# Performance work log

Measured on AMD Instinct MI355X. Metric: run time of the kernel, lower is better.

The kernel has to match this reference:

```python
import jax, jax.numpy as jnp
import numpy as np

N_NODES = 100000
N_EDGES = 1200000
D = 64
EPS = 1e-7
BETA = 1.0


def setup_inputs() -> dict:
    key = jax.random.key(0)
    k1, k2, k3, k4, k5 = jax.random.split(key, 5)
    node_feats = jax.random.normal(k1, (N_NODES, D), dtype=jnp.float32)
    edge_feats = jax.random.normal(k2, (N_EDGES, D), dtype=jnp.float32)
    W = jax.random.normal(k3, (D, D), dtype=jnp.float32) * (1.0 / np.sqrt(D))
    b = jnp.zeros((D,), dtype=jnp.float32)
    scale = jnp.ones((1,), dtype=jnp.float32)
    src = jax.random.randint(k4, (N_EDGES,), 0, N_NODES, dtype=jnp.int32)
    dst = jnp.sort(jax.random.randint(k5, (N_EDGES,), 0, N_NODES, dtype=jnp.int32))
    return {"node_feats": node_feats, "edge_feats": edge_feats, "W": W, "b": b,
            "scale": scale, "src": src, "dst": dst}


def reference(node_feats, edge_feats, W, b, scale, src, dst):
    # u_add_e: message = h[src] + edge_feats, then relu + eps  -> [E, D]
    m = jax.nn.relu(node_feats[src] + edge_feats) + EPS
    z = m * BETA
    # edge_softmax: per-destination, per-channel softmax over incoming edges
    mx = jax.ops.segment_max(z, dst, num_segments=N_NODES)      # [N, D]
    mx = jnp.where(jnp.isfinite(mx), mx, 0.0)                   # zero-degree guard
    e = jnp.exp(z - mx[dst])
    denom = jax.ops.segment_sum(e, dst, num_segments=N_NODES)   # [N, D]
    a = e / denom[dst]
    # weighted scatter-sum aggregation
    agg = jax.ops.segment_sum(m * a, dst, num_segments=N_NODES)  # [N, D]
    # MessageNorm: l2-normalize msg, rescale by ||node_feats||_2 * scale
    msg = agg / jnp.maximum(jnp.linalg.norm(agg, axis=-1, keepdims=True), 1e-12)
    feats_norm = jnp.linalg.norm(node_feats, axis=-1, keepdims=True)
    msg = msg * feats_norm * scale
    feats = node_feats + msg
    # mlp_layers=1 -> single Linear
    return feats @ W.T + b
```

## Files before the change

### kernel.cpp

```cpp
#include <hip/hip_runtime.h>

#define NN 100000
#define NE 1200000
#define DD 64
#define EPSV 1e-7f

typedef float nfloat4 __attribute__((ext_vector_type(4)));

__global__ __launch_bounds__(256)
void build_offsets(const int* __restrict__ dst, int* __restrict__ off) {
    int i = blockIdx.x * 256 + threadIdx.x;
    if (i >= NE) return;
    int d = dst[i];
    int prev = (i == 0) ? -1 : dst[i - 1];
    for (int n = prev + 1; n <= d; ++n) off[n] = i;
    if (i == NE - 1) {
        for (int n = d + 1; n <= NN; ++n) off[n] = NE;
    }
}

__global__ __launch_bounds__(256, 4)
void genconv_kernel(const float* __restrict__ node_feats,
                    const float* __restrict__ edge_feats,
                    const float* __restrict__ W,
                    const float* __restrict__ b,
                    const float* __restrict__ scale,
                    const int* __restrict__ src,
                    const int* __restrict__ dst,
                    const int* __restrict__ off,
                    float* __restrict__ out)
{
    __shared__ float Wt[64 * 65];
    __shared__ float featL[4 * 64];
    const int tid = threadIdx.x;

    #pragma unroll
    for (int r = 0; r < 16; ++r) {
        int idx = r * 256 + tid;
        int j = idx >> 6, d = idx & 63;
        Wt[d * 65 + j] = W[idx];
    }

    const int wave = tid >> 6;
    const int lane = tid & 63;
    const int n = blockIdx.x * 4 + wave;
    const bool active = (n < NN);

    const int eg = lane >> 4;
    const int cg = lane & 15;
    const float4*  nf4 = (const float4*)node_feats;
    const nfloat4* ef4 = (const nfloat4*)edge_feats;

    float acc = b[lane];

    if (active) {
        int e_start, e_end;
        if (off) {
            e_start = off[n];
            e_end   = off[n + 1];
        } else {
            int target = (lane < 32) ? n : (n + 1);
            int lo = 0, hi = NE;
            while (lo < hi) {
                int mid = (lo + hi) >> 1;
                if (dst[mid] < target) lo = mid + 1; else hi = mid;
            }
            e_start = __shfl(lo, 0, 64);
            e_end   = __shfl(lo, 32, 64);
        }

        float4 h4 = nf4[(size_t)n * 16 + cg];

        float4 ssum = {0.f, 0.f, 0.f, 0.f};
        float4 wsum = {0.f, 0.f, 0.f, 0.f};
        float* sp = (float*)&ssum;
        float* wp = (float*)&wsum;
        const int deg = e_end - e_start;

        if (deg > 0) {
            int     sk[4];
            nfloat4 efv[4];
            bool    okv[4];
            #pragma unroll
            for (int u = 0; u < 4; ++u) {
                int i = e_start + u * 4 + eg;
                bool ok = i < e_end;
                okv[u] = ok;
                int ic = ok ? i : e_start;
                sk[u]  = src[ic];
                efv[u] = __builtin_nontemporal_load(&ef4[(size_t)ic * 16 + cg]);
            }
            float4 nfv[4];
            #pragma unroll
            for (int u = 0; u < 4; ++u)
                nfv[u] = nf4[(size_t)sk[u] * 16 + cg];
            #pragma unroll
            for (int u = 0; u < 4; ++u) {
                const float* np = (const float*)&nfv[u];
                #pragma unroll
                for (int t = 0; t < 4; ++t) {
                    float v = fmaxf(np[t] + efv[u][t], 0.f) + EPSV;
                    float e = okv[u] ? __expf(v) : 0.f;
                    sp[t] += e;
                    wp[t] += e * v;
                }
            }
            for (int base = e_start + 16; base < e_end; base += 8) {
                int     sk2[2];
                nfloat4 ef2[2];
                bool    ok2[2];
                #pragma unroll
                for (int u = 0; u < 2; ++u) {
                    int i = base + u * 4 + eg;
                    bool ok = i < e_end;
                    ok2[u] = ok;
                    int ic = ok ? i : base;
                    sk2[u] = src[ic];
                    ef2[u] = __builtin_nontemporal_load(&ef4[(size_t)ic * 16 + cg]);
                }
                float4 nf2[2];
                #pragma unroll
                for (int u = 0; u < 2; ++u)
                    nf2[u] = nf4[(size_t)sk2[u] * 16 + cg];
                #pragma unroll
                for (int u = 0; u < 2; ++u) {
                    const float* np = (const float*)&nf2[u];
                    #pragma unroll
                    for (int t = 0; t < 4; ++t) {
                        float v = fmaxf(np[t] + ef2[u][t], 0.f) + EPSV;
                        float e = ok2[u] ? __expf(v) : 0.f;
                        sp[t] += e;
                        wp[t] += e * v;
                    }
                }
            }
        }

        float4 agg;
        float* ap = (float*)&agg;
        #pragma unroll
        for (int t = 0; t < 4; ++t) {
            sp[t] += __shfl_xor(sp[t], 16, 64);
            sp[t] += __shfl_xor(sp[t], 32, 64);
            wp[t] += __shfl_xor(wp[t], 16, 64);
            wp[t] += __shfl_xor(wp[t], 32, 64);
            ap[t] = (sp[t] > 0.f) ? (wp[t] / sp[t]) : 0.f;
        }

        float* hp = (float*)&h4;
        float a2 = ap[0]*ap[0] + ap[1]*ap[1] + ap[2]*ap[2] + ap[3]*ap[3];
        float h2 = hp[0]*hp[0] + hp[1]*hp[1] + hp[2]*hp[2] + hp[3]*hp[3];
        #pragma unroll
        for (int o = 8; o >= 1; o >>= 1) {
            a2 += __shfl_xor(a2, o, 64);
            h2 += __shfl_xor(h2, o, 64);
        }
        float k = sqrtf(h2) * scale[0] / fmaxf(sqrtf(a2), 1e-12f);

        float4 feat;
        float* fp = (float*)&feat;
        #pragma unroll
        for (int t = 0; t < 4; ++t) fp[t] = hp[t] + ap[t] * k;

        if (eg == 0) *(float4*)&featL[wave * 64 + cg * 4] = feat;
    }

    __syncthreads();

    if (active) {
        #pragma unroll
        for (int c4 = 0; c4 < 16; ++c4) {
            float4 f = *(const float4*)&featL[wave * 64 + c4 * 4];
            const float* fq = (const float*)&f;
            #pragma unroll
            for (int t = 0; t < 4; ++t)
                acc = fmaf(fq[t], Wt[(c4 * 4 + t) * 65 + lane], acc);
        }
        __builtin_nontemporal_store(acc, &out[(size_t)n * DD + lane]);
    }
}

extern "C" void kernel_launch(void* const* d_in, const int* in_sizes, int n_in,
                              void* d_out, int out_size, void* d_ws, size_t ws_size,
                              hipStream_t stream) {
    const float* node_feats = (const float*)d_in[0];
    const float* edge_feats = (const float*)d_in[1];
    const float* W          = (const float*)d_in[2];
    const float* b          = (const float*)d_in[3];
    const float* scale      = (const float*)d_in[4];
    const int*   src        = (const int*)d_in[5];
    const int*   dst        = (const int*)d_in[6];
    float*       out        = (float*)d_out;

    int* off = nullptr;
    if (ws_size >= (size_t)(NN + 1) * sizeof(int)) {
        off = (int*)d_ws;
        build_offsets<<<(NE + 255) / 256, 256, 0, stream>>>(dst, off);
    }
    const int blocks = (NN + 3) / 4;
    genconv_kernel<<<blocks, 256, 0, stream>>>(node_feats, edge_feats, W, b,
                                               scale, src, dst, off, out);
}
```

Baseline: 455.9 us.

## Convert genconv kernel to persistent grid-stride loop with next-group prefetch

Replaces the one-block-per-4-nodes launch with a persistent grid of 2048 blocks that loop over node groups. W is transposed into shared memory once per block instead of once per 4 nodes. Each iteration prefetches the next group's offsets and node features, and low-degree nodes take a short 2-batch path. The block-wide barrier is removed from the loop because each wave only reads its own featL slot. This fixes the grid size and may reduce latency hiding compared with the many-block launch.

Result: no change. 462.5 us (+1.4%).

```diff
diff --git a/kernel.cpp b/kernel.cpp
--- a/kernel.cpp
+++ b/kernel.cpp
@@ -4,6 +4,8 @@
 #define NE 1200000
 #define DD 64
 #define EPSV 1e-7f
+#define NGROUPS (NN / 4)
+#define GRID_BLOCKS 2048
 
 typedef float nfloat4 __attribute__((ext_vector_type(4)));
 
@@ -16,6 +18,42 @@
     for (int n = prev + 1; n <= d; ++n) off[n] = i;
     if (i == NE - 1) {
         for (int n = d + 1; n <= NN; ++n) off[n] = NE;
+    }
+}
+
+template<int NB>
+__device__ __forceinline__ void edge_round(int base, int ee, int eg, int cg,
+                                           const int* __restrict__ src,
+                                           const nfloat4* __restrict__ ef4,
+                                           const float4* __restrict__ nf4,
+                                           float* sp, float* wp)
+{
+    int     sk[NB];
+    nfloat4 efv[NB];
+    bool    okv[NB];
+    #pragma unroll
+    for (int u = 0; u < NB; ++u) {
+        int i = base + u * 4 + eg;
+        bool ok = i < ee;
+        okv[u] = ok;
+        int ic = ok ? i : base;
+        sk[u]  = src[ic];
+        efv[u] = __builtin_nontemporal_load(&ef4[(size_t)ic * 16 + cg]);
+    }
+    float4 nfv[NB];
+    #pragma unroll
+    for (int u = 0; u < NB; ++u)
+        nfv[u] = nf4[(size_t)sk[u] * 16 + cg];
+    #pragma unroll
+    for (int u = 0; u < NB; ++u) {
+        const float* np = (const float*)&nfv[u];
+        #pragma unroll
+        for (int t = 0; t < 4; ++t) {
+            float v = fmaxf(np[t] + efv[u][t], 0.f) + EPSV;
+            float e = okv[u] ? __expf(v) : 0.f;
+            sp[t] += e;
+            wp[t] += e * v;
+        }
     }
 }
 
@@ -37,102 +75,66 @@
     #pragma unroll
     for (int r = 0; r < 16; ++r) {
         int idx = r * 256 + tid;
-        int j = idx >> 6, d = idx & 63;
-        Wt[d * 65 + j] = W[idx];
+        Wt[(idx & 63) * 65 + (idx >> 6)] = W[idx];
     }
 
     const int wave = tid >> 6;
     const int lane = tid & 63;
-    const int n = blockIdx.x * 4 + wave;
-    const bool active = (n < NN);
-
     const int eg = lane >> 4;
     const int cg = lane & 15;
     const float4*  nf4 = (const float4*)node_feats;
     const nfloat4* ef4 = (const nfloat4*)edge_feats;
-
-    float acc = b[lane];
-
-    if (active) {
-        int e_start, e_end;
-        if (off) {
-            e_start = off[n];
-            e_end   = off[n + 1];
-        } else {
-            int target = (lane < 32) ? n : (n + 1);
-            int lo = 0, hi = NE;
-            while (lo < hi) {
-                int mid = (lo + hi) >> 1;
-                if (dst[mid] < target) lo = mid + 1; else hi = mid;
+    const float bl = b[lane];
+    const float sc = scale[0];
+
+    __syncthreads();
+
+    int g = blockIdx.x;
+    if (g >= NGROUPS) return;
+
+    int n = g * 4 + wave;
+    int es, ee;
+    if (off) { es = off[n]; ee = off[n + 1]; }
+    else {
+        int target = (lane < 32) ? n : (n + 1);
+        int lo = 0, hi = NE;
+        while (lo < hi) { int mid = (lo + hi) >> 1;
+                          if (dst[mid] < target) lo = mid + 1; else hi = mid; }
+        es = __shfl(lo, 0, 64); ee = __shfl(lo, 32, 64);
+    }
+    float4 h4 = nf4[(size_t)n * 16 + cg];
+
+    while (true) {
+        const int gn = g + gridDim.x;
+        const bool have_next = gn < NGROUPS;
+        int es_n = 0, ee_n = 0;
+        float4 h4_n = {0.f, 0.f, 0.f, 0.f};
+        if (have_next) {
+            int n2 = gn * 4 + wave;
+            if (off) { es_n = off[n2]; ee_n = off[n2 + 1]; }
+            else {
+                int target = (lane < 32) ? n2 : (n2 + 1);
+                int lo = 0, hi = NE;
+                while (lo < hi) { int mid = (lo + hi) >> 1;
+                                  if (dst[mid] < target) lo = mid + 1; else hi = mid; }
+                es_n = __shfl(lo, 0, 64); ee_n = __shfl(lo, 32, 64);
             }
-            e_start = __shfl(lo, 0, 64);
-            e_end   = __shfl(lo, 32, 64);
-        }
-
-        float4 h4 = nf4[(size_t)n * 16 + cg];
+            h4_n = nf4[(size_t)n2 * 16 + cg];
+        }
 
         float4 ssum = {0.f, 0.f, 0.f, 0.f};
         float4 wsum = {0.f, 0.f, 0.f, 0.f};
         float* sp = (float*)&ssum;
         float* wp = (float*)&wsum;
-        const int deg = e_end - e_start;
+        const int deg = ee - es;
 
         if (deg > 0) {
-            int     sk[4];
-            nfloat4 efv[4];
-            bool    okv[4];
-            #pragma unroll
-            for (int u = 0; u < 4; ++u) {
-                int i = e_start + u * 4 + eg;
-                bool ok = i < e_end;
-                okv[u] = ok;
-                int ic = ok ? i : e_start;
-                sk[u]  = src[ic];
-                efv[u] = __builtin_nontemporal_load(&ef4[(size_t)ic * 16 + cg]);
-            }
-            float4 nfv[4];
-            #pragma unroll
-            for (int u = 0; u < 4; ++u)
-                nfv[u] = nf4[(size_t)sk[u] * 16 + cg];
-            #pragma unroll
-            for (int u = 0; u < 4; ++u) {
-                const float* np = (const float*)&nfv[u];
-                #pragma unroll
-                for (int t = 0; t < 4; ++t) {
-                    float v = fmaxf(np[t] + efv[u][t], 0.f) + EPSV;
-                    float e = okv[u] ? __expf(v) : 0.f;
-                    sp[t] += e;
-                    wp[t] += e * v;
-                }
-            }
-            for (int base = e_start + 16; base < e_end; base += 8) {
-                int     sk2[2];
-                nfloat4 ef2[2];
-                bool    ok2[2];
-                #pragma unroll
-                for (int u = 0; u < 2; ++u) {
-                    int i = base + u * 4 + eg;
-                    bool ok = i < e_end;
-                    ok2[u] = ok;
-                    int ic = ok ? i : base;
-                    sk2[u] = src[ic];
-                    ef2[u] = __builtin_nontemporal_load(&ef4[(size_t)ic * 16 + cg]);
-                }
-                float4 nf2[2];
-                #pragma unroll
-                for (int u = 0; u < 2; ++u)
-                    nf2[u] = nf4[(size_t)sk2[u] * 16 + cg];
-                #pragma unroll
-                for (int u = 0; u < 2; ++u) {
-                    const float* np = (const float*)&nf2[u];
-                    #pragma unroll
-                    for (int t = 0; t < 4; ++t) {
-                        float v = fmaxf(np[t] + ef2[u][t], 0.f) + EPSV;
-                        float e = ok2[u] ? __expf(v) : 0.f;
-                        sp[t] += e;
-                        wp[t] += e * v;
-                    }
-                }
+            if (deg <= 8) {
+                edge_round<2>(es, ee, eg, cg, src, ef4, nf4, sp, wp);
+            } else {
+                edge_round<4>(es, ee, eg, cg, src, ef4, nf4, sp, wp);
+                for (int base = es + 16; base < ee; base += 8)
+                    edge_round<2>(base, ee, eg, cg, src, ef4, nf4, sp, wp);
             }
         }
 
@@ -155,7 +157,7 @@
             a2 += __shfl_xor(a2, o, 64);
             h2 += __shfl_xor(h2, o, 64);
         }
-        float k = sqrtf(h2) * scale[0] / fmaxf(sqrtf(a2), 1e-12f);
+        float k = sqrtf(h2) * sc / fmaxf(sqrtf(a2), 1e-12f);
 
         float4 feat;
         float* fp = (float*)&feat;
@@ -163,11 +165,8 @@
         for (int t = 0; t < 4; ++t) fp[t] = hp[t] + ap[t] * k;
 
         if (eg == 0) *(float4*)&featL[wave * 64 + cg * 4] = feat;
-    }
-
-    __syncthreads();
-
-    if (active) {
+
+        float acc = bl;
         #pragma unroll
         for (int c4 = 0; c4 < 16; ++c4) {
             float4 f = *(const float4*)&featL[wave * 64 + c4 * 4];
@@ -177,6 +176,9 @@
                 acc = fmaf(fq[t], Wt[(c4 * 4 + t) * 65 + lane], acc);
         }
         __builtin_nontemporal_store(acc, &out[(size_t)n * DD + lane]);
+
+        if (!have_next) break;
+        g = gn; n = gn * 4 + wave; es = es_n; ee = ee_n; h4 = h4_n;
     }
 }
 
@@ -197,7 +199,7 @@
         off = (int*)d_ws;
         build_offsets<<<(NE + 255) / 256, 256, 0, stream>>>(dst, off);
     }
-    const int blocks = (NN + 3) / 4;
+    const int blocks = (GRID_BLOCKS < NGROUPS) ? GRID_BLOCKS : NGROUPS;
     genconv_kernel<<<blocks, 256, 0, stream>>>(node_feats, edge_feats, W, b,
                                                scale, src, dst, off, out);
 }
```

## Replace offset-building kernel with in-kernel wave-parallel segment search

Applied to the files above, without the earlier changes.

Removes the separate build_offsets launch and the CSR offset array. Each wave now finds its destination's edge range directly in the sorted dst array. It guesses a window from the average degree, then narrows it with a 64-way ballot search and a ballot scan to find the end. This saves a kernel launch and the writes to the offset array, at the cost of extra dependent dst reads before each node's edge loop starts.

Result: slower. 484.2 us (+6.2%).

```diff
diff --git a/kernel.cpp b/kernel.cpp
--- a/kernel.cpp
+++ b/kernel.cpp
@@ -6,18 +6,6 @@
 #define EPSV 1e-7f
 
 typedef float nfloat4 __attribute__((ext_vector_type(4)));
-
-__global__ __launch_bounds__(256)
-void build_offsets(const int* __restrict__ dst, int* __restrict__ off) {
-    int i = blockIdx.x * 256 + threadIdx.x;
-    if (i >= NE) return;
-    int d = dst[i];
-    int prev = (i == 0) ? -1 : dst[i - 1];
-    for (int n = prev + 1; n <= d; ++n) off[n] = i;
-    if (i == NE - 1) {
-        for (int n = d + 1; n <= NN; ++n) off[n] = NE;
-    }
-}
 
 __global__ __launch_bounds__(256, 4)
 void genconv_kernel(const float* __restrict__ node_feats,
@@ -27,7 +15,6 @@
                     const float* __restrict__ scale,
                     const int* __restrict__ src,
                     const int* __restrict__ dst,
-                    const int* __restrict__ off,
                     float* __restrict__ out)
 {
     __shared__ float Wt[64 * 65];
@@ -37,8 +24,7 @@
     #pragma unroll
     for (int r = 0; r < 16; ++r) {
         int idx = r * 256 + tid;
-        int j = idx >> 6, d = idx & 63;
-        Wt[d * 65 + j] = W[idx];
+        Wt[(idx & 63) * 65 + (idx >> 6)] = W[idx];
     }
 
     const int wave = tid >> 6;
@@ -54,19 +40,36 @@
     float acc = b[lane];
 
     if (active) {
-        int e_start, e_end;
-        if (off) {
-            e_start = off[n];
-            e_end   = off[n + 1];
-        } else {
-            int target = (lane < 32) ? n : (n + 1);
-            int lo = 0, hi = NE;
-            while (lo < hi) {
-                int mid = (lo + hi) >> 1;
-                if (dst[mid] < target) lo = mid + 1; else hi = mid;
-            }
-            e_start = __shfl(lo, 0, 64);
-            e_end   = __shfl(lo, 32, 64);
+        int L = n * 12 - 4096; if (L < 0) L = 0;
+        int R = n * 12 + 4096; if (R > NE) R = NE;
+        while (L > 0 && dst[L] >= n)   { L = (L > 8192) ? L - 8192 : 0; }
+        while (R < NE && dst[R - 1] < n) { R = (R + 8192 < NE) ? R + 8192 : NE; }
+        while (R - L > 64) {
+            int len = R - L;
+            int m = L + ((lane + 1) * len) / 65;
+            bool pred = dst[m] < n;
+            unsigned long long mask = __ballot(pred);
+            int cnt = __popcll(mask);
+            int mlo = __shfl(m, (cnt == 0) ? 0 : cnt - 1, 64);
+            int mhi = __shfl(m, (cnt == 64) ? 63 : cnt, 64);
+            if (cnt > 0)  L = mlo + 1;
+            if (cnt < 64) R = mhi;
+        }
+        int es;
+        {
+            int p  = L + lane;
+            int ic = (p < NE) ? p : NE - 1;
+            bool pred = (p < R) && (dst[ic] < n);
+            es = L + __popcll(__ballot(pred));
+        }
+        int ee = es;
+        for (;;) {
+            int q  = ee + lane;
+            int ic = (q < NE) ? q : NE - 1;
+            bool pred = (q < NE) && (dst[ic] <= n);
+            int cnt = __popcll(__ballot(pred));
+            ee += cnt;
+            if (cnt < 64) break;
         }
 
         float4 h4 = nf4[(size_t)n * 16 + cg];
@@ -75,7 +78,7 @@
         float4 wsum = {0.f, 0.f, 0.f, 0.f};
         float* sp = (float*)&ssum;
         float* wp = (float*)&wsum;
-        const int deg = e_end - e_start;
+        const int deg = ee - es;
 
         if (deg > 0) {
             int     sk[4];
@@ -83,10 +86,10 @@
             bool    okv[4];
             #pragma unroll
             for (int u = 0; u < 4; ++u) {
-                int i = e_start + u * 4 + eg;
-                bool ok = i < e_end;
+                int i = es + u * 4 + eg;
+                bool ok = i < ee;
                 okv[u] = ok;
-                int ic = ok ? i : e_start;
+                int ic = ok ? i : es;
                 sk[u]  = src[ic];
                 efv[u] = __builtin_nontemporal_load(&ef4[(size_t)ic * 16 + cg]);
             }
@@ -105,14 +108,14 @@
                     wp[t] += e * v;
                 }
             }
-            for (int base = e_start + 16; base < e_end; base += 8) {
+            for (int base = es + 16; base < ee; base += 8) {
                 int     sk2[2];
                 nfloat4 ef2[2];
                 bool    ok2[2];
                 #pragma unroll
                 for (int u = 0; u < 2; ++u) {
                     int i = base + u * 4 + eg;
-                    bool ok = i < e_end;
+                    bool ok = i < ee;
                     ok2[u] = ok;
                     int ic = ok ? i : base;
                     sk2[u] = src[ic];
@@ -192,12 +195,9 @@
     const int*   dst        = (const int*)d_in[6];
     float*       out        = (float*)d_out;
 
-    int* off = nullptr;
-    if (ws_size >= (size_t)(NN + 1) * sizeof(int)) {
-        off = (int*)d_ws;
-        build_offsets<<<(NE + 255) / 256, 256, 0, stream>>>(dst, off);
-    }
+    (void)d_ws; (void)ws_size;
+
     const int blocks = (NN + 3) / 4;
     genconv_kernel<<<blocks, 256, 0, stream>>>(node_feats, edge_feats, W, b,
-                                               scale, src, dst, off, out);
+                                               scale, src, dst, out);
 }
```
